# Performance work log

Hardware: AMD Instinct MI355X
Metric: run time of the kernel (lower is better)

Reference implementation:

```python
import jax, jax.numpy as jnp
import numpy as np
from jax import lax

RADIUS = 0.15
K = 32          # num_neighbors
S = 1024        # num_centers
GROUPS = 8      # GroupNorm groups
EPS = 1e-5


def furthest_point_sample(xyz, n_samples):
    # xyz: [B, N, 3] -> indices [B, n_samples] (sequential FPS, start at index 0)
    B, N, _ = xyz.shape
    def step(carry, _):
        min_d, far = carry                      # [B,N], [B]
        sel = jnp.take_along_axis(xyz, far[:, None, None], axis=1)  # [B,1,3]
        d = jnp.sum((xyz - sel) ** 2, axis=-1)  # [B,N]
        min_d = jnp.minimum(min_d, d)
        nxt = jnp.argmax(min_d, axis=-1).astype(jnp.int32)
        return (min_d, nxt), far
    init = (jnp.full((B, N), jnp.inf, dtype=xyz.dtype), jnp.zeros((B,), jnp.int32))
    _, idxs = lax.scan(step, init, None, length=n_samples)  # [n_samples, B]
    return idxs.T  # [B, n_samples]


def ball_query(centers, points, radius, k):
    # centers: [B,3,S], points: [B,3,N] -> neighbor indices [B,S,k]
    B = points.shape[0]
    N = points.shape[-1]
    d2 = jnp.sum((centers[:, :, :, None] - points[:, :, None, :]) ** 2, axis=1)  # [B,S,N]
    valid = d2 < radius * radius
    order = jnp.where(valid, jnp.arange(N, dtype=jnp.int32), jnp.int32(N))
    topk = jnp.sort(order, axis=-1)[..., :k]            # first-k in-ball indices (CUDA ball_query order)
    first = topk[..., :1]
    idx = jnp.where(topk < N, topk, first)              # pad shortfall with first in-ball point
    idx = jnp.where(idx == N, 0, idx)                   # empty ball -> index 0
    return idx


def grouping(x, idx):
    # x: [B,C,N], idx: [B,S,k] -> [B,C,S,k]
    B, C, N = x.shape
    _, s, k = idx.shape
    flat = idx.reshape(B, 1, s * k)
    g = jnp.take_along_axis(x, jnp.broadcast_to(flat, (B, C, s * k)), axis=2)
    return g.reshape(B, C, s, k)


def group_norm(x, gamma, beta):
    # x: [B,C,S,K], GroupNorm(GROUPS)
    B, C, s, k = x.shape
    xg = x.reshape(B, GROUPS, C // GROUPS, s, k)
    mu = jnp.mean(xg, axis=(2, 3, 4), keepdims=True)
    var = jnp.var(xg, axis=(2, 3, 4), keepdims=True)
    xn = ((xg - mu) * lax.rsqrt(var + EPS)).reshape(B, C, s, k)
    return xn * gamma[None, :, None, None] + beta[None, :, None, None]


def mlp_layer(x, w, b, gamma, beta):
    # 1x1 Conv2d + GroupNorm + swish; x: [B,C,S,K], w: [O,C]
    y = jnp.einsum('bcsk,oc->bosk', x, w) + b[None, :, None, None]
    y = group_norm(y, gamma, beta)
    return y * jax.nn.sigmoid(y)


def setup_inputs() -> dict:
    key = jax.random.key(0)
    ks = jax.random.split(key, 20)
    B, C_IN, N = 8, 128, 4096
    features = jax.random.normal(ks[0], (B, C_IN, N), jnp.float32)
    coords = jax.random.uniform(ks[1], (B, 3, N), jnp.float32)
    time_emb = jax.random.normal(ks[2], (B, 64, N), jnp.float32)
    style = jax.random.normal(ks[3], (B, 64), jnp.float32)
    chans = [C_IN + 3, 128, 128, 256]
    inp = dict(features=features, coords=coords, time_emb=time_emb, style=style)
    for i in range(3):
        ci, co = chans[i], chans[i + 1]
        inp[f'w{i+1}'] = jax.random.normal(ks[4 + 4 * i], (co, ci), jnp.float32) / np.sqrt(ci)
        inp[f'b{i+1}'] = jnp.zeros((co,), jnp.float32)
        inp[f'g{i+1}'] = jnp.ones((co,), jnp.float32)
        inp[f'be{i+1}'] = jnp.zeros((co,), jnp.float32)
    return inp


def reference(features, coords, time_emb, style,
              w1, b1, g1, be1, w2, b2, g2, be2, w3, b3, g3, be3):
    # FPS -> center coords
    fps_idx = furthest_point_sample(coords.transpose(0, 2, 1), S)       # [B,S]
    B = coords.shape[0]
    centers = jnp.take_along_axis(coords, jnp.broadcast_to(fps_idx[:, None, :], (B, 3, S)), axis=2)  # [B,3,S]
    # Ball query + grouping (include_coordinates=True)
    nidx = ball_query(centers, coords, RADIUS, K)                       # [B,S,K]
    ncoords = grouping(coords, nidx) - centers[:, :, :, None]           # [B,3,S,K]
    nfeat = jnp.concatenate([ncoords, grouping(features, nidx)], axis=1)  # [B,3+C,S,K]
    # SharedMLP (1x1 conv + GN(8) + swish) x3, then max over neighbors
    x = mlp_layer(nfeat, w1, b1, g1, be1)
    x = mlp_layer(x, w2, b2, g2, be2)
    x = mlp_layer(x, w3, b3, g3, be3)
    out = jnp.max(x, axis=-1)                                           # [B,256,S]
    return out, centers, time_emb[:, :, :S], style
```

## Files before the change

kernel.cpp:

```cpp
#include <hip/hip_runtime.h>
#include <hip/hip_bf16.h>

#define BATCH 8
#define NPTS 4096
#define NS   1024
#define NK   32
#define CIN  128
#define C1PAD 160
#define O1   128
#define O3   256
#define MTOT 32768
#define GN_EPS 1e-5f
#define SREP 16

typedef float f32x4 __attribute__((ext_vector_type(4)));
typedef float f32x2 __attribute__((ext_vector_type(2)));
typedef short s16x8 __attribute__((ext_vector_type(8)));
typedef short s16x4 __attribute__((ext_vector_type(4)));
typedef unsigned long long u64;
typedef u64 u64x2 __attribute__((ext_vector_type(2)));

static __device__ __forceinline__ unsigned short f2bf(float f){
  unsigned u = __float_as_uint(f);
  u += 0x7fffu + ((u >> 16) & 1u);
  return (unsigned short)(u >> 16);
}
static __device__ __forceinline__ float bf2f(unsigned short h){
  return __uint_as_float(((unsigned)h) << 16);
}
static __device__ __forceinline__ float exact_d2(float ax,float ay,float az,float bx,float by,float bz){
  float dx=__fadd_rn(ax,-bx), dy=__fadd_rn(ay,-by), dz=__fadd_rn(az,-bz);
  return __fadd_rn(__fadd_rn(__fmul_rn(dx,dx),__fmul_rn(dy,dy)),__fmul_rn(dz,dz));
}
static __device__ __forceinline__ unsigned wave_umax_dpp(unsigned v){
  unsigned o;
  o = (unsigned)__builtin_amdgcn_update_dpp(0, (int)v, 0x111, 0xf, 0xf, true); v = (o>v)?o:v;
  o = (unsigned)__builtin_amdgcn_update_dpp(0, (int)v, 0x112, 0xf, 0xf, true); v = (o>v)?o:v;
  o = (unsigned)__builtin_amdgcn_update_dpp(0, (int)v, 0x114, 0xf, 0xf, true); v = (o>v)?o:v;
  o = (unsigned)__builtin_amdgcn_update_dpp(0, (int)v, 0x118, 0xf, 0xf, true); v = (o>v)?o:v;
  o = (unsigned)__builtin_amdgcn_update_dpp(0, (int)v, 0x142, 0xf, 0xf, true); v = (o>v)?o:v;
  o = (unsigned)__builtin_amdgcn_update_dpp(0, (int)v, 0x143, 0xf, 0xf, true); v = (o>v)?o:v;
  return v;
}
static __device__ __forceinline__ float wave_fsum_dpp(float v){
  int o;
  o=__builtin_amdgcn_update_dpp(0,__float_as_int(v),0x111,0xf,0xf,true); v+=__int_as_float(o);
  o=__builtin_amdgcn_update_dpp(0,__float_as_int(v),0x112,0xf,0xf,true); v+=__int_as_float(o);
  o=__builtin_amdgcn_update_dpp(0,__float_as_int(v),0x114,0xf,0xf,true); v+=__int_as_float(o);
  o=__builtin_amdgcn_update_dpp(0,__float_as_int(v),0x118,0xf,0xf,true); v+=__int_as_float(o);
  o=__builtin_amdgcn_update_dpp(0,__float_as_int(v),0x142,0xf,0xf,true); v+=__int_as_float(o);
  o=__builtin_amdgcn_update_dpp(0,__float_as_int(v),0x143,0xf,0xf,true); v+=__int_as_float(o);
  return v;
}
static __device__ __forceinline__ float fast_sigmoid(float x){
  return __builtin_amdgcn_rcpf(1.0f + __expf(-x));
}
static __device__ __forceinline__ void stats_sum(const float* __restrict__ stats,
                                                 int layer,int b,int g,float& s1,float& s2){
  const float* p = stats + (size_t)(((layer*BATCH+b)*8+g)*SREP)*2;
  float a=0.f, q=0.f;
  #pragma unroll
  for(int r=0;r<SREP;++r){ a+=p[r*2]; q+=p[r*2+1]; }
  s1=a; s2=q;
}

#define FPS_BLOCKS 8
#define FT_BASE    8
#define FT_BLOCKS  128
#define ZP_BASE    136
#define ZP_BLOCKS  8
#define WP_BASE    144
#define WP_BLOCKS  58
#define MS_BASE    202
#define MS_BLOCKS  32
#define TOTAL_BLOCKS 234
#define WP_TASKS   (8704 + 3*BATCH*8*SREP*2)

__global__ __launch_bounds__(256) void k_fused(
    const float* __restrict__ coords, const float* __restrict__ features,
    const float* __restrict__ time_emb, const float* __restrict__ style,
    const float* __restrict__ w1, const float* __restrict__ w2, const float* __restrict__ w3,
    float* __restrict__ centers, float* __restrict__ out_time, float* __restrict__ out_style,
    unsigned short* __restrict__ featT, unsigned short* __restrict__ wfrag,
    float* __restrict__ stats){
  union U {
    struct { float4 lc[NPTS];
             unsigned long long red[2][4] __attribute__((aligned(16)));
             float cx_[NS]; float cy_[NS]; float cz_[NS]; } fps;
    float tile[64][65];
  };
  __shared__ U sm;
  const int blk = blockIdx.x;
  const int t = threadIdx.x;

  if(blk < FPS_BLOCKS){
    const int b = blk;
    const float* cb = coords + (size_t)b*3*NPTS;
    const int lane = t & 63, wid = t >> 6;
    f32x2 px2[8],py2[8],pz2[8],md2[8];
    #pragma unroll
    for(int i=0;i<8;++i){
      int p0 = t + (2*i)*256;
      px2[i]=(f32x2){cb[p0],cb[p0+256]};
      py2[i]=(f32x2){cb[NPTS+p0],cb[NPTS+p0+256]};
      pz2[i]=(f32x2){cb[2*NPTS+p0],cb[2*NPTS+p0+256]};
      md2[i]=(f32x2){3.4e38f,3.4e38f};
      sm.fps.lc[p0]     = make_float4(px2[i].x, py2[i].x, pz2[i].x, 0.f);
      sm.fps.lc[p0+256] = make_float4(px2[i].y, py2[i].y, pz2[i].y, 0.f);
    }
    float ax=cb[0], ay=cb[NPTS], az=cb[2*NPTS];
    if(t==0){ sm.fps.cx_[0]=ax; sm.fps.cy_[0]=ay; sm.fps.cz_[0]=az; }
    __syncthreads();
    for(int it=1; it<NS; ++it){
      {
        #pragma clang fp contract(off)
        f32x2 axv={ax,ax}, ayv={ay,ay}, azv={az,az};
        #pragma unroll
        for(int i=0;i<8;++i){
          f32x2 dx=px2[i]-axv, dy=py2[i]-ayv, dz=pz2[i]-azv;
          f32x2 d = dx*dx + dy*dy + dz*dz;
          md2[i]=__builtin_elementwise_min(md2[i],d);
        }
      }
      f32x2 t01=__builtin_elementwise_max(md2[0],md2[1]);
      f32x2 t23=__builtin_elementwise_max(md2[2],md2[3]);
      f32x2 t45=__builtin_elementwise_max(md2[4],md2[5]);
      f32x2 t67=__builtin_elementwise_max(md2[6],md2[7]);
      f32x2 ta=__builtin_elementwise_max(t01,t23);
      f32x2 tb=__builtin_elementwise_max(t45,t67);
      f32x2 tc=__builtin_elementwise_max(ta,tb);
      float bmax=fmaxf(tc.x,tc.y);
      unsigned bvb=(unsigned)__builtin_amdgcn_readlane((int)wave_umax_dpp(__float_as_uint(bmax)),63);
      unsigned cand=0u;
      #pragma unroll
      for(int s=15;s>=0;--s){
        float mv = (s&1)? md2[s>>1].y : md2[s>>1].x;
        cand = (__float_as_uint(mv)==bvb) ? ~(unsigned)(s*256+t) : cand;
      }
      unsigned mc = wave_umax_dpp(cand);
      const int buf=it&1;
      if(lane==63) sm.fps.red[buf][wid] = ((u64)bvb<<32) | mc;
      __syncthreads();
      u64x2 r0 = *(const u64x2*)&sm.fps.red[buf][0];
      u64x2 r1 = *(const u64x2*)&sm.fps.red[buf][2];
      u64 a0 = r0.x>r0.y?r0.x:r0.y;
      u64 a1 = r1.x>r1.y?r1.x:r1.y;
      u64 w  = a0>a1?a0:a1;
      unsigned idx = ~(unsigned)w;
      float4 c4 = sm.fps.lc[idx];
      ax=c4.x; ay=c4.y; az=c4.z;
      if(t==0){ sm.fps.cx_[it]=ax; sm.fps.cy_[it]=ay; sm.fps.cz_[it]=az; }
    }
    __syncthreads();
    for(int i=t;i<NS;i+=256){
      centers[(size_t)(b*3+0)*NS+i]=sm.fps.cx_[i];
      centers[(size_t)(b*3+1)*NS+i]=sm.fps.cy_[i];
      centers[(size_t)(b*3+2)*NS+i]=sm.fps.cz_[i];
    }
    return;
  }

  if(blk < ZP_BASE){
    const int pb = blk - FT_BASE;
    for(int j=0;j<8;++j){
      int tid = pb*8 + j;
      int bb = tid>>7, r = tid&127, ct = r>>6, pt = r&63;
      int c0 = ct*64, p0 = pt*64;
      #pragma unroll
      for(int i=0;i<16;++i){
        int c = (t>>6)*16 + i;
        sm.tile[c][t&63] = features[((size_t)bb*CIN + c0 + c)*NPTS + p0 + (t&63)];
      }
      __syncthreads();
      #pragma unroll
      for(int i=0;i<16;++i){
        int pl = (t>>6)*16 + i;
        featT[((size_t)bb*NPTS + p0 + pl)*C1PAD + c0 + (t&63)] = f2bf(sm.tile[t&63][pl]);
      }
      __syncthreads();
    }
    return;
  }

  if(blk < WP_BASE){
    const int zb = blk - ZP_BASE;
    s16x8 z = (s16x8){0,0,0,0,0,0,0,0};
    #pragma unroll 4
    for(int i=0;i<64;++i){
      int q = zb*16384 + i*256 + t;
      int bb = q>>14, rem = q&16383, r = rem>>2, c8 = (rem&3)*8;
      *(s16x8*)&featT[((size_t)bb*NPTS + r)*C1PAD + 128 + c8] = z;
    }
    return;
  }

  if(blk < MS_BASE){
    int task = (blk - WP_BASE)*256 + t;
    if(task >= WP_TASKS) return;
    if(task >= 8704){
      stats[task - 8704] = 0.f;
      return;
    }
    int layer, of, cs, ln, ncs; size_t base;
    if(task < 2560){ layer=0; ncs=5; base=0;     int r=task;      of=r/320; r%=320; cs=r>>6; ln=r&63; }
    else if(task < 4608){ layer=1; ncs=4; base=20480; int r=task-2560; of=r>>8; r&=255; cs=r>>6; ln=r&63; }
    else { layer=2; ncs=4; base=36864; int r=task-4608; of=r>>8; r&=255; cs=r>>6; ln=r&63; }
    int o = of*16 + (ln&15);
    s16x8 vals;
    #pragma unroll
    for(int i=0;i<8;++i){
      int c = cs*32 + (ln>>4)*8 + i;
      float v = 0.f;
      if(layer==0){
        if(c<128) v = w1[o*131 + c + 3];
        else if(c<131) v = w1[o*131 + (c-128)];
      } else if(layer==1){
        if(c<128) v = w2[o*128 + c];
      } else {
        if(c<128) v = w3[o*128 + c];
      }
      vals[i]=(short)f2bf(v);
    }
    *(s16x8*)&wfrag[base + ((size_t)(of*ncs + cs)*64 + ln)*8] = vals;
    return;
  }

  {
    const int mb = blk - MS_BASE;
    #pragma unroll 4
    for(int i=0;i<16;++i){
      int q = mb*4096 + i*256 + t;
      int f = q*4;
      int bb = f>>16, c = (f>>10)&63, s = f&1023;
      *(float4*)&out_time[f] = *(const float4*)&time_emb[((size_t)bb*64 + c)*NPTS + s];
    }
    if(mb==0){ out_style[t]=style[t]; out_style[256+t]=style[256+t]; }
  }
}

__global__ __launch_bounds__(256) void k_ballq(const float* __restrict__ coords,
                                               const float* __restrict__ centers,
                                               int* __restrict__ nidx){
  const int gw = (blockIdx.x*256 + threadIdx.x) >> 6;
  const int lane = threadIdx.x & 63;
  const int wl = (threadIdx.x >> 6);
  const int b = gw >> 10, s = gw & (NS-1);
  const float* cb = coords + (size_t)b*3*NPTS;
  const float cx = centers[(size_t)(b*3+0)*NS+s];
  const float cy = centers[(size_t)(b*3+1)*NS+s];
  const float cz = centers[(size_t)(b*3+2)*NS+s];
  __shared__ int slots[4][NK];
  int cnt = 0;
  for(int base=0; base<NPTS && cnt<NK; base+=64){
    int p = base + lane;
    float d2 = exact_d2(cb[p], cb[NPTS+p], cb[2*NPTS+p], cx,cy,cz);
    bool valid = d2 < 0.0225f;
    unsigned long long mask = __ballot(valid);
    int pos = cnt + (int)__popcll(mask & ((1ull<<lane)-1ull));
    if(valid && pos < NK) slots[wl][pos] = p;
    cnt += (int)__popcll(mask);
  }
  __syncthreads();
  int first = slots[wl][0];
  if(lane < NK){
    int v = (lane < cnt) ? slots[wl][lane] : first;
    nidx[((size_t)b*NS + s)*NK + lane] = v;
  }
}

__global__ __launch_bounds__(256) void k_gemm1(const unsigned short* __restrict__ featT,
    const int* __restrict__ nidx, const float* __restrict__ coords,
    const float* __restrict__ centers, const unsigned short* __restrict__ wfrag,
    const float* __restrict__ bias, unsigned short* __restrict__ yout,
    float* __restrict__ stats){
  const int b=blockIdx.y, mt=blockIdx.x;
  const int m0=mt*64;
  const int t=threadIdx.x, lane=t&63, wid=t>>6;
  __shared__ unsigned short xs[64][168];
  __shared__ unsigned short ys[64][136];
  __shared__ int pidx[64];
  __shared__ float cenS[2][3];
  __shared__ float wsum[2][8][4];
  if(t<64) pidx[t]=nidx[(size_t)b*MTOT + m0 + t];
  if(t>=64 && t<70){ int u=t-64; int j=u/3, c=u%3; cenS[j][c]=centers[((size_t)b*3+c)*NS + (m0>>5)+j]; }
  __syncthreads();
  for(int q=t;q<1280;q+=256){
    int r=q&63, ch=q>>6;
    *(s16x8*)&xs[r][ch*8] = *(const s16x8*)&featT[((size_t)b*NPTS + pidx[r])*C1PAD + ch*8];
  }
  __syncthreads();
  if(t<64){
    int p=pidx[t]; int sj=t>>5;
    float n0=__fadd_rn(coords[((size_t)b*3+0)*NPTS+p],-cenS[sj][0]);
    float n1=__fadd_rn(coords[((size_t)b*3+1)*NPTS+p],-cenS[sj][1]);
    float n2=__fadd_rn(coords[((size_t)b*3+2)*NPTS+p],-cenS[sj][2]);
    s16x4 nc={(short)f2bf(n0),(short)f2bf(n1),(short)f2bf(n2),0};
    *(s16x4*)&xs[t][128]=nc;
  }
  __syncthreads();
  f32x4 acc[8];
  #pragma unroll
  for(int i=0;i<8;++i) acc[i]=(f32x4){0.f,0.f,0.f,0.f};
  const unsigned short* xrow=&xs[wid*16+(lane&15)][0];
  #pragma unroll
  for(int cs=0;cs<5;++cs){
    s16x8 bfv=*(const s16x8*)&xrow[cs*32+(lane>>4)*8];
    #pragma unroll
    for(int of=0;of<8;++of){
      s16x8 afv=*(const s16x8*)&wfrag[((size_t)(of*5+cs)*64+lane)*8];
      acc[of]=__builtin_amdgcn_mfma_f32_16x16x32_bf16(afv,bfv,acc[of],0,0,0);
    }
  }
  #pragma unroll
  for(int of=0;of<8;++of){
    float ls=0.f,lq=0.f;
    int obase=of*16+((lane>>4)<<2);
    #pragma unroll
    for(int r=0;r<4;++r){
      float y=acc[of][r]+bias[obase+r];
      ys[wid*16+(lane&15)][obase+r]=f2bf(y);
      ls+=y; lq+=y*y;
    }
    ls=wave_fsum_dpp(ls); lq=wave_fsum_dpp(lq);
    if(lane==63){ wsum[0][of][wid]=ls; wsum[1][of][wid]=lq; }
  }
  __syncthreads();
  for(int q=t;q<1024;q+=256){
    int r=q&63, ch=q>>6;
    *(s16x8*)&yout[((size_t)b*MTOT+m0+r)*O1 + ch*8] = *(const s16x8*)&ys[r][ch*8];
  }
  if(t<8){
    float s1v=wsum[0][t][0]+wsum[0][t][1]+wsum[0][t][2]+wsum[0][t][3];
    float s2v=wsum[1][t][0]+wsum[1][t][1]+wsum[1][t][2]+wsum[1][t][3];
    int rep = mt & (SREP-1);
    atomicAdd(&stats[(((0*BATCH+b)*8+t)*SREP+rep)*2+0],s1v);
    atomicAdd(&stats[(((0*BATCH+b)*8+t)*SREP+rep)*2+1],s2v);
  }
}

template<int LAYER>
__global__ __launch_bounds__(256) void k_gemm23(const unsigned short* __restrict__ xin,
    const unsigned short* __restrict__ wfrag, const float* __restrict__ bias,
    const float* __restrict__ stats, const float* __restrict__ gprev,
    const float* __restrict__ beprev, unsigned short* __restrict__ yout,
    float* __restrict__ ymm, float* __restrict__ statsOut){
  const int b=blockIdx.y, mt=blockIdx.x;
  const int m0=mt*64;
  const int t=threadIdx.x, lane=t&63, wid=t>>6;
  __shared__ unsigned short xs[64][136];
  __shared__ unsigned short ys[64][136];
  __shared__ float lsc[CIN], lsh[CIN];
  __shared__ float wsum[2][8][4];
  if(t<CIN){
    int g = t>>4;
    const float cnt = 16.0f*NS*NK;
    float s1,s2; stats_sum(stats, LAYER-1, b, g, s1, s2);
    float mu=s1/cnt, var=s2/cnt-mu*mu;
    float sc=gprev[t]*rsqrtf(var+GN_EPS);
    lsc[t]=sc; lsh[t]=beprev[t]-mu*sc;
  }
  __syncthreads();
  for(int q=t;q<1024;q+=256){
    int r=q&63, ch=q>>6;
    s16x8 v = *(const s16x8*)&xin[((size_t)b*MTOT + m0 + r)*CIN + ch*8];
    s16x8 o;
    #pragma unroll
    for(int i=0;i<8;++i){
      int c=ch*8+i;
      float x = bf2f((unsigned short)v[i]);
      x = x*lsc[c] + lsh[c];
      o[i]=(short)f2bf(x*fast_sigmoid(x));
    }
    *(s16x8*)&xs[r][ch*8]=o;
  }
  __syncthreads();
  const unsigned short* xrow=&xs[wid*16+(lane&15)][0];
  s16x8 bfv[4];
  #pragma unroll
  for(int cs=0;cs<4;++cs) bfv[cs]=*(const s16x8*)&xrow[cs*32+(lane>>4)*8];
  const int NPH=(LAYER==2)?2:1;
  #pragma unroll
  for(int ph=0; ph<NPH; ++ph){
    f32x4 acc[8];
    #pragma unroll
    for(int i=0;i<8;++i) acc[i]=(f32x4){0.f,0.f,0.f,0.f};
    #pragma unroll
    for(int cs=0;cs<4;++cs){
      #pragma unroll
      for(int of=0;of<8;++of){
        int ofg=ph*8+of;
        s16x8 afv=*(const s16x8*)&wfrag[((size_t)(ofg*4+cs)*64+lane)*8];
        acc[of]=__builtin_amdgcn_mfma_f32_16x16x32_bf16(afv,bfv[cs],acc[of],0,0,0);
      }
    }
    #pragma unroll
    for(int of=0;of<8;++of){
      float ls=0.f,lq=0.f;
      int lobase=of*16+((lane>>4)<<2);
      #pragma unroll
      for(int r=0;r<4;++r){
        float y=acc[of][r]+bias[ph*128+lobase+r];
        ys[wid*16+(lane&15)][lobase+r]=f2bf(y);
        ls+=y; lq+=y*y;
      }
      ls=wave_fsum_dpp(ls); lq=wave_fsum_dpp(lq);
      if(lane==63){ wsum[0][of][wid]=ls; wsum[1][of][wid]=lq; }
    }
    __syncthreads();
    if constexpr(LAYER==1){
      for(int q=t;q<1024;q+=256){
        int r=q&63, ch=q>>6;
        *(s16x8*)&yout[((size_t)b*MTOT+m0+r)*O1 + ch*8] = *(const s16x8*)&ys[r][ch*8];
      }
    } else {
      int c = t&127, sg = t>>7;
      float mn=3.4e38f, mx=-3.4e38f;
      #pragma unroll 8
      for(int k=0;k<32;++k){
        float v = bf2f(ys[sg*32+k][c]);
        mn=fminf(mn,v); mx=fmaxf(mx,v);
      }
      *(float2*)&ymm[(((size_t)b*NS + mt*2 + sg)*512) + (size_t)(ph*128+c)*2] = make_float2(mn,mx);
    }
    if(t<8){
      float s1v=wsum[0][t][0]+wsum[0][t][1]+wsum[0][t][2]+wsum[0][t][3];
      float s2v=wsum[1][t][0]+wsum[1][t][1]+wsum[1][t][2]+wsum[1][t][3];
      int g = (LAYER==2) ? (ph*4 + (t>>1)) : t;
      int rep = mt & (SREP-1);
      atomicAdd(&statsOut[(((LAYER*BATCH+b)*8+g)*SREP+rep)*2+0],s1v);
      atomicAdd(&statsOut[(((LAYER*BATCH+b)*8+g)*SREP+rep)*2+1],s2v);
    }
    if(ph+1<NPH) __syncthreads();
  }
}

__global__ __launch_bounds__(256) void k_out(const float* __restrict__ ymm,
    const float* __restrict__ stats, const float* __restrict__ g3,
    const float* __restrict__ be3, float* __restrict__ out){
  const int b=blockIdx.z, st=blockIdx.x;
  const int t=threadIdx.x;
  __shared__ float outT[256][33];
  const int c=t, g=c>>5;
  const float cnt = 32.0f*NS*NK;
  float s1,s2; stats_sum(stats, 2, b, g, s1, s2);
  float mu=s1/cnt, var=s2/cnt-mu*mu;
  float sc=g3[c]*rsqrtf(var+GN_EPS);
  float sh=be3[c]-mu*sc;
  for(int si=0;si<32;++si){
    int s=st*32+si;
    float2 v=*(const float2*)&ymm[((size_t)b*NS+s)*512 + (size_t)c*2];
    float za=v.x*sc+sh, zb=v.y*sc+sh;
    float fa=za*fast_sigmoid(za);
    float fb=zb*fast_sigmoid(zb);
    outT[c][si]=fmaxf(fa,fb);
  }
  __syncthreads();
  #pragma unroll
  for(int i=0;i<32;++i){
    int row=(t>>5)+i*8;
    out[((size_t)(b*256+row))*NS + st*32 + (t&31)] = outT[row][t&31];
  }
}

extern "C" void kernel_launch(void* const* d_in, const int* in_sizes, int n_in,
                              void* d_out, int out_size, void* d_ws, size_t ws_size,
                              hipStream_t stream){
  const float* features=(const float*)d_in[0];
  const float* coords=(const float*)d_in[1];
  const float* time_emb=(const float*)d_in[2];
  const float* style=(const float*)d_in[3];
  const float* w1=(const float*)d_in[4];
  const float* b1=(const float*)d_in[5];
  const float* g1=(const float*)d_in[6];
  const float* be1=(const float*)d_in[7];
  const float* w2=(const float*)d_in[8];
  const float* b2=(const float*)d_in[9];
  const float* g2=(const float*)d_in[10];
  const float* be2=(const float*)d_in[11];
  const float* w3=(const float*)d_in[12];
  const float* b3=(const float*)d_in[13];
  const float* g3=(const float*)d_in[14];
  const float* be3=(const float*)d_in[15];

  float* out0=(float*)d_out;
  float* out_centers=out0 + (size_t)BATCH*O3*NS;
  float* out_time=out_centers + (size_t)BATCH*3*NS;
  float* out_style=out_time + (size_t)BATCH*64*NS;

  char* ws=(char*)d_ws;
  int* nidx=(int*)(ws + 131072);
  unsigned short* featT=(unsigned short*)(ws + 1179648);
  unsigned short* wfrag=(unsigned short*)(ws + 11796480);
  float* stats=(float*)(ws + 11939840);
  float* ymm=(float*)(ws + 12582912);
  unsigned short* y1=(unsigned short*)(ws + 33554432);
  unsigned short* y2=(unsigned short*)(ws + 100663296);

  k_fused<<<TOTAL_BLOCKS,256,0,stream>>>(coords,features,time_emb,style,w1,w2,w3,
                                         out_centers,out_time,out_style,featT,wfrag,stats);
  k_ballq<<<2048,256,0,stream>>>(coords,out_centers,nidx);
  k_gemm1<<<dim3(512,BATCH),256,0,stream>>>(featT,nidx,coords,out_centers,wfrag,b1,y1,stats);
  k_gemm23<1><<<dim3(512,BATCH),256,0,stream>>>(y1,wfrag+20480,b2,stats,g1,be1,y2,ymm,stats);
  k_gemm23<2><<<dim3(512,BATCH),256,0,stream>>>(y2,wfrag+36864,b3,stats,g2,be2,y2,ymm,stats);
  k_out<<<dim3(32,1,BATCH),256,0,stream>>>(ymm,stats,g3,be3,out0);
}
```

Measured before the change: 894.6 us.

## Run FPS on a single wavefront to drop per-iteration block barriers

The furthest-point-sampling blocks now run on one 64-lane wavefront that holds all 4096 points in registers (64 per lane). This removes the shared-memory cross-wave reduction and the __syncthreads on each of the 1024 sequential iterations, replacing them with DPP wave reductions and readlane. Each iteration now does four times more per-lane arithmetic, register pressure rises, and three of the four waves in each FPS block sit idle. Separately, the stats replication factor grows from 16 to 64 with more weight-prep blocks, and the stats summation reads float2 pairs.

```diff
diff --git a/kernel.cpp b/kernel.cpp
--- a/kernel.cpp
+++ b/kernel.cpp
@@ -11,7 +11,7 @@
 #define O3   256
 #define MTOT 32768
 #define GN_EPS 1e-5f
-#define SREP 16
+#define SREP 64
 
 typedef float f32x4 __attribute__((ext_vector_type(4)));
 typedef float f32x2 __attribute__((ext_vector_type(2)));
@@ -57,10 +57,10 @@
 }
 static __device__ __forceinline__ void stats_sum(const float* __restrict__ stats,
                                                  int layer,int b,int g,float& s1,float& s2){
-  const float* p = stats + (size_t)(((layer*BATCH+b)*8+g)*SREP)*2;
+  const float2* p = (const float2*)(stats + (size_t)(((layer*BATCH+b)*8+g)*SREP)*2);
   float a=0.f, q=0.f;
   #pragma unroll
-  for(int r=0;r<SREP;++r){ a+=p[r*2]; q+=p[r*2+1]; }
+  for(int r=0;r<SREP;++r){ float2 v=p[r]; a+=v.x; q+=v.y; }
   s1=a; s2=q;
 }
 
@@ -70,10 +70,10 @@
 #define ZP_BASE    136
 #define ZP_BLOCKS  8
 #define WP_BASE    144
-#define WP_BLOCKS  58
-#define MS_BASE    202
+#define WP_BLOCKS  130
+#define MS_BASE    274
 #define MS_BLOCKS  32
-#define TOTAL_BLOCKS 234
+#define TOTAL_BLOCKS 306
 #define WP_TASKS   (8704 + 3*BATCH*8*SREP*2)
 
 __global__ __launch_bounds__(256) void k_fused(
@@ -85,7 +85,6 @@
     float* __restrict__ stats){
   union U {
     struct { float4 lc[NPTS];
-             unsigned long long red[2][4] __attribute__((aligned(16)));
              float cx_[NS]; float cy_[NS]; float cz_[NS]; } fps;
     float tile[64][65];
   };
@@ -95,64 +94,68 @@
 
   if(blk < FPS_BLOCKS){
     const int b = blk;
+    if(t >= 64) return;
+    const int lane = t;
     const float* cb = coords + (size_t)b*3*NPTS;
-    const int lane = t & 63, wid = t >> 6;
-    f32x2 px2[8],py2[8],pz2[8],md2[8];
-    #pragma unroll
-    for(int i=0;i<8;++i){
-      int p0 = t + (2*i)*256;
-      px2[i]=(f32x2){cb[p0],cb[p0+256]};
-      py2[i]=(f32x2){cb[NPTS+p0],cb[NPTS+p0+256]};
-      pz2[i]=(f32x2){cb[2*NPTS+p0],cb[2*NPTS+p0+256]};
+    f32x2 px2[32],py2[32],pz2[32],md2[32];
+    #pragma unroll
+    for(int i=0;i<32;++i){
+      int p0 = lane + (2*i)*64;
+      px2[i]=(f32x2){cb[p0],cb[p0+64]};
+      py2[i]=(f32x2){cb[NPTS+p0],cb[NPTS+p0+64]};
+      pz2[i]=(f32x2){cb[2*NPTS+p0],cb[2*NPTS+p0+64]};
       md2[i]=(f32x2){3.4e38f,3.4e38f};
-      sm.fps.lc[p0]     = make_float4(px2[i].x, py2[i].x, pz2[i].x, 0.f);
-      sm.fps.lc[p0+256] = make_float4(px2[i].y, py2[i].y, pz2[i].y, 0.f);
+      sm.fps.lc[p0]    = make_float4(px2[i].x, py2[i].x, pz2[i].x, 0.f);
+      sm.fps.lc[p0+64] = make_float4(px2[i].y, py2[i].y, pz2[i].y, 0.f);
     }
     float ax=cb[0], ay=cb[NPTS], az=cb[2*NPTS];
-    if(t==0){ sm.fps.cx_[0]=ax; sm.fps.cy_[0]=ay; sm.fps.cz_[0]=az; }
-    __syncthreads();
+    if(lane==0){ sm.fps.cx_[0]=ax; sm.fps.cy_[0]=ay; sm.fps.cz_[0]=az; }
     for(int it=1; it<NS; ++it){
       {
         #pragma clang fp contract(off)
         f32x2 axv={ax,ax}, ayv={ay,ay}, azv={az,az};
         #pragma unroll
-        for(int i=0;i<8;++i){
+        for(int i=0;i<32;++i){
           f32x2 dx=px2[i]-axv, dy=py2[i]-ayv, dz=pz2[i]-azv;
           f32x2 d = dx*dx + dy*dy + dz*dz;
           md2[i]=__builtin_elementwise_min(md2[i],d);
         }
       }
-      f32x2 t01=__builtin_elementwise_max(md2[0],md2[1]);
-      f32x2 t23=__builtin_elementwise_max(md2[2],md2[3]);
-      f32x2 t45=__builtin_elementwise_max(md2[4],md2[5]);
-      f32x2 t67=__builtin_elementwise_max(md2[6],md2[7]);
-      f32x2 ta=__builtin_elementwise_max(t01,t23);
-      f32x2 tb=__builtin_elementwise_max(t45,t67);
-      f32x2 tc=__builtin_elementwise_max(ta,tb);
-      float bmax=fmaxf(tc.x,tc.y);
+      f32x2 l1[16];
+      #pragma unroll
+      for(int i=0;i<16;++i) l1[i]=__builtin_elementwise_max(md2[2*i],md2[2*i+1]);
+      f32x2 l2[8];
+      #pragma unroll
+      for(int i=0;i<8;++i) l2[i]=__builtin_elementwise_max(l1[2*i],l1[2*i+1]);
+      f32x2 l3[4];
+      #pragma unroll
+      for(int i=0;i<4;++i) l3[i]=__builtin_elementwise_max(l2[2*i],l2[2*i+1]);
+      f32x2 l4a=__builtin_elementwise_max(l3[0],l3[1]);
+      f32x2 l4b=__builtin_elementwise_max(l3[2],l3[3]);
+      f32x2 l5=__builtin_elementwise_max(l4a,l4b);
+      float bmax=fmaxf(l5.x,l5.y);
       unsigned bvb=(unsigned)__builtin_amdgcn_readlane((int)wave_umax_dpp(__float_as_uint(bmax)),63);
-      unsigned cand=0u;
+      unsigned c0=0u,c1=0u,c2=0u,c3=0u;
       #pragma unroll
       for(int s=15;s>=0;--s){
-        float mv = (s&1)? md2[s>>1].y : md2[s>>1].x;
-        cand = (__float_as_uint(mv)==bvb) ? ~(unsigned)(s*256+t) : cand;
-      }
+        int h=s>>1; int odd=s&1;
+        float v0 = odd? md2[h].y    : md2[h].x;
+        float v1 = odd? md2[8+h].y  : md2[8+h].x;
+        float v2 = odd? md2[16+h].y : md2[16+h].x;
+        float v3 = odd? md2[24+h].y : md2[24+h].x;
+        c0 = (__float_as_uint(v0)==bvb)? ~(unsigned)((s   )*64+lane) : c0;
+        c1 = (__float_as_uint(v1)==bvb)? ~(unsigned)((16+s)*64+lane) : c1;
+        c2 = (__float_as_uint(v2)==bvb)? ~(unsigned)((32+s)*64+lane) : c2;
+        c3 = (__float_as_uint(v3)==bvb)? ~(unsigned)((48+s)*64+lane) : c3;
+      }
+      unsigned cand = c0? c0 : (c1? c1 : (c2? c2 : c3));
       unsigned mc = wave_umax_dpp(cand);
-      const int buf=it&1;
-      if(lane==63) sm.fps.red[buf][wid] = ((u64)bvb<<32) | mc;
-      __syncthreads();
-      u64x2 r0 = *(const u64x2*)&sm.fps.red[buf][0];
-      u64x2 r1 = *(const u64x2*)&sm.fps.red[buf][2];
-      u64 a0 = r0.x>r0.y?r0.x:r0.y;
-      u64 a1 = r1.x>r1.y?r1.x:r1.y;
-      u64 w  = a0>a1?a0:a1;
-      unsigned idx = ~(unsigned)w;
+      unsigned idx = ~(unsigned)__builtin_amdgcn_readlane((int)mc,63);
       float4 c4 = sm.fps.lc[idx];
       ax=c4.x; ay=c4.y; az=c4.z;
-      if(t==0){ sm.fps.cx_[it]=ax; sm.fps.cy_[it]=ay; sm.fps.cz_[it]=az; }
-    }
-    __syncthreads();
-    for(int i=t;i<NS;i+=256){
+      if(lane==0){ sm.fps.cx_[it]=ax; sm.fps.cy_[it]=ay; sm.fps.cz_[it]=az; }
+    }
+    for(int i=lane;i<NS;i+=64){
       centers[(size_t)(b*3+0)*NS+i]=sm.fps.cx_[i];
       centers[(size_t)(b*3+1)*NS+i]=sm.fps.cy_[i];
       centers[(size_t)(b*3+2)*NS+i]=sm.fps.cz_[i];
```

New measurement: 1.789 ms. 2x slower.
